# Optimization experiments

Hardware: AMD Instinct MI355X
Metric: run time of the kernel (lower is better)

Reference implementation:

```python
import jax, jax.numpy as jnp
import numpy as np

N_UE = 100000
N_AP = 10000
N_E = 1600000
D = 64
H = 128


def setup_inputs() -> dict:
    key = jax.random.key(0)
    ks = jax.random.split(key, 10)
    s = 0.05
    return {
        "ue_hid": jax.random.normal(ks[0], (N_UE, D), jnp.float32),
        "ap_hid": jax.random.normal(ks[1], (N_AP, D), jnp.float32),
        "edge_hid": jax.random.normal(ks[2], (N_E, D), jnp.float32),
        "src": jax.random.randint(ks[3], (N_E,), 0, N_UE),
        "dst": jax.random.randint(ks[4], (N_E,), 0, N_AP),
        "W1a": jax.random.normal(ks[5], (2 * D, H), jnp.float32) * s,
        "b1a": jnp.zeros((H,), jnp.float32),
        "W1b": jax.random.normal(ks[6], (H, H), jnp.float32) * s,
        "b1b": jnp.zeros((H,), jnp.float32),
        "W2a": jax.random.normal(ks[7], (D + H, H), jnp.float32) * s,
        "b2a": jnp.zeros((H,), jnp.float32),
        "W2b": jax.random.normal(ks[8], (H, D), jnp.float32) * s,
        "b2b": jnp.zeros((D,), jnp.float32),
    }


def reference(ue_hid, ap_hid, edge_hid, src, dst,
              W1a, b1a, W1b, b1b, W2a, b2a, W2b, b2b):
    # message: concat(edge_feature, src UE feature) -> [E, 2D]
    msg = jnp.concatenate([edge_hid, ue_hid[src]], axis=-1)
    # mlp1 applied per edge (DGL applies it inside reduce on the mailbox,
    # which is equivalent to per-edge application followed by segment sum)
    h = jnp.maximum(msg @ W1a + b1a, 0.0) @ W1b + b1b          # [E, H]
    # sum over mailbox (all edges with the same destination AP)
    agg = jax.ops.segment_sum(h, dst, num_segments=N_AP)        # [N_AP, H]
    # mlp2 on concat(AP hid, aggregated messages)
    z = jnp.concatenate([ap_hid, agg], axis=-1)                 # [N_AP, D+H]
    new_ap = jnp.maximum(z @ W2a + b2a, 0.0) @ W2b + b2b        # [N_AP, D]
    return new_ap
```

## Files before the change

### kernel.cpp

```cpp
#include <hip/hip_runtime.h>
#include <hip/hip_bf16.h>

#define N_UE 100000
#define N_AP 10000
#define N_E  1600000
#define DD   64
#define HH   128

typedef float f32x4 __attribute__((ext_vector_type(4)));
typedef short s8b   __attribute__((ext_vector_type(8)));
typedef short s4b   __attribute__((ext_vector_type(4)));

static __device__ __forceinline__ unsigned short f2bf(float x) {
  union { float f; unsigned int u; } v; v.f = x;
  unsigned int r = v.u + 0x7fffu + ((v.u >> 16) & 1u);
  return (unsigned short)(r >> 16);
}

__global__ void apk0_prep(const float* __restrict__ W1a, short* __restrict__ WTg,
                          int* __restrict__ counts, float* __restrict__ aggW) {
  int i = blockIdx.x * 256 + threadIdx.x;
  int n = gridDim.x * 256;
  for (int x = i; x < 128 * 128; x += n) {
    int col = x >> 7, k = x & 127;
    WTg[x] = (short)f2bf(W1a[k * 128 + col]);
  }
  for (int x = i; x < N_AP; x += n) counts[x] = 0;
  for (int x = i; x < N_AP * 128 / 4; x += n)
    ((float4*)aggW)[x] = make_float4(0.f, 0.f, 0.f, 0.f);
}

__global__ void apk2_hist(const int* __restrict__ dst, int* __restrict__ counts) {
  int i = blockIdx.x * blockDim.x + threadIdx.x;
  int stride = gridDim.x * blockDim.x;
  for (; i < N_E; i += stride) atomicAdd(&counts[dst[i]], 1);
}

__global__ __launch_bounds__(256) void apk3_scan(const int* __restrict__ counts,
                                                 int* __restrict__ offsets,
                                                 int* __restrict__ cursor) {
  __shared__ int p[256];
  int t = threadIdx.x;
  const int CH = 40;
  int start = t * CH, end = min(start + CH, N_AP);
  int s = 0;
  for (int i = start; i < end; i++) s += counts[i];
  p[t] = s;
  __syncthreads();
  for (int d = 1; d < 256; d <<= 1) {
    int v = p[t] + ((t >= d) ? p[t - d] : 0);
    __syncthreads();
    p[t] = v;
    __syncthreads();
  }
  int base = (t == 0) ? 0 : p[t - 1];
  for (int i = start; i < end; i++) {
    offsets[i] = base;
    cursor[i] = base;
    base += counts[i];
  }
  if (t == 255) offsets[N_AP] = base;
}

__global__ void apk4_scatter(const int* __restrict__ dst, const int* __restrict__ src,
                             int* __restrict__ cursor, int4* __restrict__ triple) {
  int i = blockIdx.x * blockDim.x + threadIdx.x;
  int stride = gridDim.x * blockDim.x;
  for (; i < N_E; i += stride) {
    int d = dst[i];
    int pos = atomicAdd(&cursor[d], 1);
    triple[pos] = make_int4(i, src[i], d, 0);
  }
}

__global__ __launch_bounds__(256, 2) void apk5_edges(
    const float* __restrict__ edge_hid, const float* __restrict__ ue_hid,
    const short* __restrict__ WTg, const float* __restrict__ b1a,
    const int4* __restrict__ triple, float* __restrict__ aggW) {
  __shared__ short WT[128][140];
  __shared__ short A[128][140];
  __shared__ int eids[128];
  __shared__ int usrc[128];
  __shared__ int segs[128];
  int t = threadIdx.x, blk = blockIdx.x;
  int wave = t >> 6, lane = t & 63, quad = lane >> 4, l16 = lane & 15;

  if (t < 128) {
    int4 tr = triple[(size_t)blk * 128 + t];
    eids[t] = tr.x; usrc[t] = tr.y; segs[t] = tr.z;
  }
  for (int i = t; i < 2048; i += 256) {
    int col = i >> 4, seg16 = i & 15;
    *(s8b*)&WT[col][seg16 * 8] = ((const s8b*)WTg)[i];
  }
  __syncthreads();

  {
    int r = t >> 1, h = t & 1;
    const float* srow = h ? (ue_hid + (size_t)usrc[r] * 64)
                          : (edge_hid + (size_t)eids[r] * 64);
    int kb = h * 64;
    for (int cc = 0; cc < 8; cc++) {
      float4 v = ((const float4*)srow)[cc * 2];
      float4 w = ((const float4*)srow)[cc * 2 + 1];
      s8b p;
      p[0] = (short)f2bf(v.x); p[1] = (short)f2bf(v.y);
      p[2] = (short)f2bf(v.z); p[3] = (short)f2bf(v.w);
      p[4] = (short)f2bf(w.x); p[5] = (short)f2bf(w.y);
      p[6] = (short)f2bf(w.z); p[7] = (short)f2bf(w.w);
      *(s8b*)&A[r][kb + cc * 8] = p;
    }
  }
  __syncthreads();

  s8b bf[2][4];
  for (int ct = 0; ct < 2; ct++)
    for (int ks = 0; ks < 4; ks++)
      bf[ct][ks] = *(const s8b*)&WT[wave * 32 + ct * 16 + l16][ks * 32 + quad * 8];
  float bias0 = b1a[wave * 32 + l16];
  float bias1 = b1a[wave * 32 + 16 + l16];

  int runseg = segs[0];
  float run0 = 0.f, run1 = 0.f;
  for (int rt = 0; rt < 8; rt++) {
    s8b a0 = *(const s8b*)&A[rt * 16 + l16][quad * 8];
    s8b a1 = *(const s8b*)&A[rt * 16 + l16][32 + quad * 8];
    s8b a2 = *(const s8b*)&A[rt * 16 + l16][64 + quad * 8];
    s8b a3 = *(const s8b*)&A[rt * 16 + l16][96 + quad * 8];
    f32x4 c0 = {0.f, 0.f, 0.f, 0.f}, c1 = {0.f, 0.f, 0.f, 0.f};
    c0 = __builtin_amdgcn_mfma_f32_16x16x32_bf16(a0, bf[0][0], c0, 0, 0, 0);
    c0 = __builtin_amdgcn_mfma_f32_16x16x32_bf16(a1, bf[0][1], c0, 0, 0, 0);
    c0 = __builtin_amdgcn_mfma_f32_16x16x32_bf16(a2, bf[0][2], c0, 0, 0, 0);
    c0 = __builtin_amdgcn_mfma_f32_16x16x32_bf16(a3, bf[0][3], c0, 0, 0, 0);
    c1 = __builtin_amdgcn_mfma_f32_16x16x32_bf16(a0, bf[1][0], c1, 0, 0, 0);
    c1 = __builtin_amdgcn_mfma_f32_16x16x32_bf16(a1, bf[1][1], c1, 0, 0, 0);
    c1 = __builtin_amdgcn_mfma_f32_16x16x32_bf16(a2, bf[1][2], c1, 0, 0, 0);
    c1 = __builtin_amdgcn_mfma_f32_16x16x32_bf16(a3, bf[1][3], c1, 0, 0, 0);
    int sj[4]; float t0[4], t1[4];
    for (int j = 0; j < 4; j++) {
      int gr = rt * 16 + quad * 4 + j;
      sj[j] = segs[gr];
      t0[j] = fmaxf(c0[j] + bias0, 0.f);
      t1[j] = fmaxf(c1[j] + bias1, 0.f);
    }
    int s0 = segs[rt * 16], s1 = segs[rt * 16 + 15];
    for (int s = s0; s <= s1; s++) {
      float v0 = 0.f, v1 = 0.f;
      for (int j = 0; j < 4; j++)
        if (sj[j] == s) { v0 += t0[j]; v1 += t1[j]; }
      v0 += __shfl_xor(v0, 16); v0 += __shfl_xor(v0, 32);
      v1 += __shfl_xor(v1, 16); v1 += __shfl_xor(v1, 32);
      if (s == runseg) { run0 += v0; run1 += v1; }
      else {
        if (quad == 0) {
          atomicAdd(&aggW[(size_t)runseg * 128 + wave * 32 + l16], run0);
          atomicAdd(&aggW[(size_t)runseg * 128 + wave * 32 + 16 + l16], run1);
        }
        runseg = s; run0 = v0; run1 = v1;
      }
    }
  }
  if (quad == 0) {
    atomicAdd(&aggW[(size_t)runseg * 128 + wave * 32 + l16], run0);
    atomicAdd(&aggW[(size_t)runseg * 128 + wave * 32 + 16 + l16], run1);
  }
}

__global__ __launch_bounds__(256) void apk6_mlp2(
    const float* __restrict__ ap_hid, const float* __restrict__ W1b,
    const float* __restrict__ b1b, const float* __restrict__ W2a,
    const float* __restrict__ b2a, const float* __restrict__ W2b,
    const float* __restrict__ b2b, const float* __restrict__ aggW,
    const int* __restrict__ offsets, float* __restrict__ out) {
  __shared__ float wbuf[64 * 128];
  __shared__ float zrows[16 * 128];
  __shared__ float yrows[16 * 128];
  __shared__ float arows[16 * 64];
  __shared__ float cbuf[16];
  int t = threadIdx.x;
  int apb = blockIdx.x * 16;
  for (int i = t; i < 16 * 128 / 4; i += 256)
    ((float4*)zrows)[i] = ((const float4*)(aggW + (size_t)apb * 128))[i];
  for (int i = t; i < 16 * 64 / 4; i += 256)
    ((float4*)arows)[i] = ((const float4*)(ap_hid + (size_t)apb * 64))[i];
  if (t < 16) cbuf[t] = (float)(offsets[apb + t + 1] - offsets[apb + t]);
  int j = t & 127, half = t >> 7;
  {
    float bb = b1b[j];
    __syncthreads();
    float acc[8];
    for (int r = 0; r < 8; r++) acc[r] = cbuf[half * 8 + r] * bb;
    for (int p = 0; p < 2; p++) {
      __syncthreads();
      for (int i = t; i < 64 * 128 / 4; i += 256)
        ((float4*)wbuf)[i] = ((const float4*)(W1b + p * 64 * 128))[i];
      __syncthreads();
      for (int k = 0; k < 64; k++) {
        float w = wbuf[k * 128 + j];
        for (int r = 0; r < 8; r++)
          acc[r] += zrows[(half * 8 + r) * 128 + (p * 64 + k)] * w;
      }
    }
    for (int r = 0; r < 8; r++) yrows[(half * 8 + r) * 128 + j] = acc[r];
  }
  {
    float acc2[8];
    float bb = b2a[j];
    for (int r = 0; r < 8; r++) acc2[r] = bb;
    __syncthreads();
    for (int i = t; i < 64 * 128 / 4; i += 256)
      ((float4*)wbuf)[i] = ((const float4*)W2a)[i];
    __syncthreads();
    for (int k = 0; k < 64; k++) {
      float w = wbuf[k * 128 + j];
      for (int r = 0; r < 8; r++) acc2[r] += arows[(half * 8 + r) * 64 + k] * w;
    }
    for (int p = 0; p < 2; p++) {
      __syncthreads();
      for (int i = t; i < 64 * 128 / 4; i += 256)
        ((float4*)wbuf)[i] = ((const float4*)(W2a + (64 + p * 64) * 128))[i];
      __syncthreads();
      for (int k = 0; k < 64; k++) {
        float w = wbuf[k * 128 + j];
        for (int r = 0; r < 8; r++)
          acc2[r] += yrows[(half * 8 + r) * 128 + (p * 64 + k)] * w;
      }
    }
    __syncthreads();
    for (int r = 0; r < 8; r++)
      zrows[(half * 8 + r) * 128 + j] = fmaxf(acc2[r], 0.f);
  }
  {
    __syncthreads();
    for (int i = t; i < 128 * 64 / 4; i += 256)
      ((float4*)wbuf)[i] = ((const float4*)W2b)[i];
    __syncthreads();
    int i2 = t & 63, q = t >> 6;
    float acc3[4];
    float bb = b2b[i2];
    for (int r = 0; r < 4; r++) acc3[r] = bb;
    for (int k = 0; k < 128; k++) {
      float w = wbuf[k * 64 + i2];
      for (int r = 0; r < 4; r++) acc3[r] += zrows[(q * 4 + r) * 128 + k] * w;
    }
    for (int r = 0; r < 4; r++)
      out[(size_t)(apb + q * 4 + r) * 64 + i2] = acc3[r];
  }
}

extern "C" void kernel_launch(void* const* d_in, const int* in_sizes, int n_in,
                              void* d_out, int out_size, void* d_ws, size_t ws_size,
                              hipStream_t stream) {
  const float* ue_hid   = (const float*)d_in[0];
  const float* ap_hid   = (const float*)d_in[1];
  const float* edge_hid = (const float*)d_in[2];
  const int*   src      = (const int*)d_in[3];
  const int*   dst      = (const int*)d_in[4];
  const float* W1a      = (const float*)d_in[5];
  const float* b1a      = (const float*)d_in[6];
  const float* W1b      = (const float*)d_in[7];
  const float* b1b      = (const float*)d_in[8];
  const float* W2a      = (const float*)d_in[9];
  const float* b2a      = (const float*)d_in[10];
  const float* W2b      = (const float*)d_in[11];
  const float* b2b      = (const float*)d_in[12];
  float* out = (float*)d_out;

  unsigned char* ws = (unsigned char*)d_ws;
  short* WTg    = (short*)(ws);
  int* counts   = (int*)(ws + 32768);
  int* offsets  = (int*)(ws + 73728);
  int* cursor   = (int*)(ws + 114688);
  float* aggW   = (float*)(ws + 155648);
  int4* triple  = (int4*)(ws + 5275648);

  apk0_prep<<<640, 256, 0, stream>>>(W1a, WTg, counts, aggW);
  apk2_hist<<<2048, 256, 0, stream>>>(dst, counts);
  apk3_scan<<<1, 256, 0, stream>>>(counts, offsets, cursor);
  apk4_scatter<<<2048, 256, 0, stream>>>(dst, src, cursor, triple);
  apk5_edges<<<N_E / 128, 256, 0, stream>>>(edge_hid, ue_hid, WTg, b1a, triple, aggW);
  apk6_mlp2<<<N_AP / 16, 256, 0, stream>>>(ap_hid, W1b, b1b, W2a, b2a, W2b, b2b,
                                           aggW, offsets, out);
}
```

Before: 947.3 us.

## Make edge kernel persistent with register-resident weights and deferred shuffle reduction

The edge-MLP kernel becomes a grid-stride persistent kernel over 128-edge tiles, launched with 2048 blocks. The W1a B-fragments are now loaded once per block from global memory straight into registers, so the shared-memory weight tile goes away. LDS use drops and launch bounds rise to 4 blocks per CU. The segment reduction adds a fast path for row-tiles that fall in a single destination and moves the cross-quad shuffles into the flush, so they run once per segment change rather than per segment per tile. This cuts per-block setup and shuffle overhead, at the cost of tighter register limits and two barriers per tile in the persistent loop.

```diff
diff --git a/kernel.cpp b/kernel.cpp
--- a/kernel.cpp
+++ b/kernel.cpp
@@ -6,6 +6,7 @@
 #define N_E  1600000
 #define DD   64
 #define HH   128
+#define NTILE (N_E / 128)
 
 typedef float f32x4 __attribute__((ext_vector_type(4)));
 typedef short s8b   __attribute__((ext_vector_type(8)));
@@ -73,97 +74,101 @@
   }
 }
 
-__global__ __launch_bounds__(256, 2) void apk5_edges(
+__global__ __launch_bounds__(256, 4) void apk5_edges(
     const float* __restrict__ edge_hid, const float* __restrict__ ue_hid,
     const short* __restrict__ WTg, const float* __restrict__ b1a,
     const int4* __restrict__ triple, float* __restrict__ aggW) {
-  __shared__ short WT[128][140];
-  __shared__ short A[128][140];
-  __shared__ int eids[128];
-  __shared__ int usrc[128];
+  __shared__ short A[128][132];
   __shared__ int segs[128];
-  int t = threadIdx.x, blk = blockIdx.x;
+  int t = threadIdx.x;
   int wave = t >> 6, lane = t & 63, quad = lane >> 4, l16 = lane & 15;
-
-  if (t < 128) {
-    int4 tr = triple[(size_t)blk * 128 + t];
-    eids[t] = tr.x; usrc[t] = tr.y; segs[t] = tr.z;
-  }
-  for (int i = t; i < 2048; i += 256) {
-    int col = i >> 4, seg16 = i & 15;
-    *(s8b*)&WT[col][seg16 * 8] = ((const s8b*)WTg)[i];
-  }
-  __syncthreads();
-
-  {
-    int r = t >> 1, h = t & 1;
-    const float* srow = h ? (ue_hid + (size_t)usrc[r] * 64)
-                          : (edge_hid + (size_t)eids[r] * 64);
-    int kb = h * 64;
-    for (int cc = 0; cc < 8; cc++) {
-      float4 v = ((const float4*)srow)[cc * 2];
-      float4 w = ((const float4*)srow)[cc * 2 + 1];
-      s8b p;
-      p[0] = (short)f2bf(v.x); p[1] = (short)f2bf(v.y);
-      p[2] = (short)f2bf(v.z); p[3] = (short)f2bf(v.w);
-      p[4] = (short)f2bf(w.x); p[5] = (short)f2bf(w.y);
-      p[6] = (short)f2bf(w.z); p[7] = (short)f2bf(w.w);
-      *(s8b*)&A[r][kb + cc * 8] = p;
-    }
-  }
-  __syncthreads();
 
   s8b bf[2][4];
   for (int ct = 0; ct < 2; ct++)
     for (int ks = 0; ks < 4; ks++)
-      bf[ct][ks] = *(const s8b*)&WT[wave * 32 + ct * 16 + l16][ks * 32 + quad * 8];
+      bf[ct][ks] = *(const s8b*)&WTg[(wave * 32 + ct * 16 + l16) * 128 +
+                                     ks * 32 + quad * 8];
   float bias0 = b1a[wave * 32 + l16];
   float bias1 = b1a[wave * 32 + 16 + l16];
 
-  int runseg = segs[0];
+  int runseg = -1;
   float run0 = 0.f, run1 = 0.f;
-  for (int rt = 0; rt < 8; rt++) {
-    s8b a0 = *(const s8b*)&A[rt * 16 + l16][quad * 8];
-    s8b a1 = *(const s8b*)&A[rt * 16 + l16][32 + quad * 8];
-    s8b a2 = *(const s8b*)&A[rt * 16 + l16][64 + quad * 8];
-    s8b a3 = *(const s8b*)&A[rt * 16 + l16][96 + quad * 8];
-    f32x4 c0 = {0.f, 0.f, 0.f, 0.f}, c1 = {0.f, 0.f, 0.f, 0.f};
-    c0 = __builtin_amdgcn_mfma_f32_16x16x32_bf16(a0, bf[0][0], c0, 0, 0, 0);
-    c0 = __builtin_amdgcn_mfma_f32_16x16x32_bf16(a1, bf[0][1], c0, 0, 0, 0);
-    c0 = __builtin_amdgcn_mfma_f32_16x16x32_bf16(a2, bf[0][2], c0, 0, 0, 0);
-    c0 = __builtin_amdgcn_mfma_f32_16x16x32_bf16(a3, bf[0][3], c0, 0, 0, 0);
-    c1 = __builtin_amdgcn_mfma_f32_16x16x32_bf16(a0, bf[1][0], c1, 0, 0, 0);
-    c1 = __builtin_amdgcn_mfma_f32_16x16x32_bf16(a1, bf[1][1], c1, 0, 0, 0);
-    c1 = __builtin_amdgcn_mfma_f32_16x16x32_bf16(a2, bf[1][2], c1, 0, 0, 0);
-    c1 = __builtin_amdgcn_mfma_f32_16x16x32_bf16(a3, bf[1][3], c1, 0, 0, 0);
-    int sj[4]; float t0[4], t1[4];
-    for (int j = 0; j < 4; j++) {
-      int gr = rt * 16 + quad * 4 + j;
-      sj[j] = segs[gr];
-      t0[j] = fmaxf(c0[j] + bias0, 0.f);
-      t1[j] = fmaxf(c1[j] + bias1, 0.f);
-    }
-    int s0 = segs[rt * 16], s1 = segs[rt * 16 + 15];
-    for (int s = s0; s <= s1; s++) {
-      float v0 = 0.f, v1 = 0.f;
-      for (int j = 0; j < 4; j++)
-        if (sj[j] == s) { v0 += t0[j]; v1 += t1[j]; }
-      v0 += __shfl_xor(v0, 16); v0 += __shfl_xor(v0, 32);
-      v1 += __shfl_xor(v1, 16); v1 += __shfl_xor(v1, 32);
-      if (s == runseg) { run0 += v0; run1 += v1; }
-      else {
-        if (quad == 0) {
-          atomicAdd(&aggW[(size_t)runseg * 128 + wave * 32 + l16], run0);
-          atomicAdd(&aggW[(size_t)runseg * 128 + wave * 32 + 16 + l16], run1);
+  auto flush = [&]() {
+    if (runseg >= 0) {
+      float f0 = run0 + __shfl_xor(run0, 16); f0 += __shfl_xor(f0, 32);
+      float f1 = run1 + __shfl_xor(run1, 16); f1 += __shfl_xor(f1, 32);
+      if (quad == 0) {
+        atomicAdd(&aggW[(size_t)runseg * 128 + wave * 32 + l16], f0);
+        atomicAdd(&aggW[(size_t)runseg * 128 + wave * 32 + 16 + l16], f1);
+      }
+    }
+  };
+
+  const int r = t >> 1, h = t & 1;
+  for (int tile = blockIdx.x; tile < NTILE; tile += gridDim.x) {
+    int4 tr = triple[(size_t)tile * 128 + r];
+    __syncthreads();
+    if (h == 0) segs[r] = tr.z;
+    {
+      const float* srow = h ? (ue_hid + (size_t)tr.y * 64)
+                            : (edge_hid + (size_t)tr.x * 64);
+      int kb = h * 64;
+      #pragma unroll
+      for (int cc = 0; cc < 8; cc++) {
+        float4 v = ((const float4*)srow)[cc * 2];
+        float4 w = ((const float4*)srow)[cc * 2 + 1];
+        s8b p;
+        p[0] = (short)f2bf(v.x); p[1] = (short)f2bf(v.y);
+        p[2] = (short)f2bf(v.z); p[3] = (short)f2bf(v.w);
+        p[4] = (short)f2bf(w.x); p[5] = (short)f2bf(w.y);
+        p[6] = (short)f2bf(w.z); p[7] = (short)f2bf(w.w);
+        *(s8b*)&A[r][kb + cc * 8] = p;
+      }
+    }
+    __syncthreads();
+
+    for (int rt = 0; rt < 8; rt++) {
+      s8b a0 = *(const s8b*)&A[rt * 16 + l16][0 + quad * 8];
+      s8b a1 = *(const s8b*)&A[rt * 16 + l16][32 + quad * 8];
+      s8b a2 = *(const s8b*)&A[rt * 16 + l16][64 + quad * 8];
+      s8b a3 = *(const s8b*)&A[rt * 16 + l16][96 + quad * 8];
+      f32x4 c0 = {0.f, 0.f, 0.f, 0.f}, c1 = {0.f, 0.f, 0.f, 0.f};
+      c0 = __builtin_amdgcn_mfma_f32_16x16x32_bf16(a0, bf[0][0], c0, 0, 0, 0);
+      c0 = __builtin_amdgcn_mfma_f32_16x16x32_bf16(a1, bf[0][1], c0, 0, 0, 0);
+      c0 = __builtin_amdgcn_mfma_f32_16x16x32_bf16(a2, bf[0][2], c0, 0, 0, 0);
+      c0 = __builtin_amdgcn_mfma_f32_16x16x32_bf16(a3, bf[0][3], c0, 0, 0, 0);
+      c1 = __builtin_amdgcn_mfma_f32_16x16x32_bf16(a0, bf[1][0], c1, 0, 0, 0);
+      c1 = __builtin_amdgcn_mfma_f32_16x16x32_bf16(a1, bf[1][1], c1, 0, 0, 0);
+      c1 = __builtin_amdgcn_mfma_f32_16x16x32_bf16(a2, bf[1][2], c1, 0, 0, 0);
+      c1 = __builtin_amdgcn_mfma_f32_16x16x32_bf16(a3, bf[1][3], c1, 0, 0, 0);
+      float t0[4], t1[4];
+      #pragma unroll
+      for (int j = 0; j < 4; j++) {
+        t0[j] = fmaxf(c0[j] + bias0, 0.f);
+        t1[j] = fmaxf(c1[j] + bias1, 0.f);
+      }
+      int gb = rt * 16;
+      int sF = segs[gb], sL = segs[gb + 15];
+      if (sF == sL) {
+        if (sF != runseg) { flush(); runseg = sF; run0 = 0.f; run1 = 0.f; }
+        run0 += t0[0] + t0[1] + t0[2] + t0[3];
+        run1 += t1[0] + t1[1] + t1[2] + t1[3];
+      } else {
+        int sj[4];
+        #pragma unroll
+        for (int j = 0; j < 4; j++) sj[j] = segs[gb + quad * 4 + j];
+        for (int s = sF; s <= sL; s++) {
+          float v0 = 0.f, v1 = 0.f;
+          #pragma unroll
+          for (int j = 0; j < 4; j++)
+            if (sj[j] == s) { v0 += t0[j]; v1 += t1[j]; }
+          if (s == runseg) { run0 += v0; run1 += v1; }
+          else { flush(); runseg = s; run0 = v0; run1 = v1; }
         }
-        runseg = s; run0 = v0; run1 = v1;
-      }
-    }
-  }
-  if (quad == 0) {
-    atomicAdd(&aggW[(size_t)runseg * 128 + wave * 32 + l16], run0);
-    atomicAdd(&aggW[(size_t)runseg * 128 + wave * 32 + 16 + l16], run1);
-  }
+      }
+    }
+  }
+  flush();
 }
 
 __global__ __launch_bounds__(256) void apk6_mlp2(
@@ -278,7 +283,7 @@
   apk2_hist<<<2048, 256, 0, stream>>>(dst, counts);
   apk3_scan<<<1, 256, 0, stream>>>(counts, offsets, cursor);
   apk4_scatter<<<2048, 256, 0, stream>>>(dst, src, cursor, triple);
-  apk5_edges<<<N_E / 128, 256, 0, stream>>>(edge_hid, ue_hid, WTg, b1a, triple, aggW);
+  apk5_edges<<<2048, 256, 0, stream>>>(edge_hid, ue_hid, WTg, b1a, triple, aggW);
   apk6_mlp2<<<N_AP / 16, 256, 0, stream>>>(ap_hid, W1b, b1b, W2a, b2a, W2b, b2b,
                                            aggW, offsets, out);
 }
```

Result: faster. 914.3 us (-3.5%).
